# Kernel optimization log

Measured on AMD Instinct MI355X. Metric: run time of the kernel, lower is better.

Reference implementation:

```python
import jax, jax.numpy as jnp
import numpy as np

D = 64  # hidden size

def _ffn2(x, w1, b1, w2, b2):
    # Linear -> ReLU -> Linear (no activation after last layer, matching FFN)
    return jax.nn.relu(x @ w1 + b1) @ w2 + b2

def setup_inputs() -> dict:
    key = jax.random.key(0)
    ks = jax.random.split(key, 40)
    B, NP, NY, NO = 512, 128, 1024, 256
    f32 = jnp.float32
    def n(k, sh, s=0.1):
        return (jax.random.normal(k, sh) * s).astype(f32)
    inp = {
        'pred_state': jax.random.normal(ks[0], (B, NP, 2), dtype=f32),
        'prey_state': jax.random.normal(ks[1], (B, NY, 2), dtype=f32),
        'obst_state': jax.random.normal(ks[2], (B, NO, 3), dtype=f32),
        'prey_is_alive': jax.random.randint(ks[3], (B, NY), 0, 2).astype(bool),
        'emb': n(ks[4], (3, D)),
        'e0_w1': n(ks[5], (2, D)), 'e0_b1': n(ks[6], (D,)),
        'e0_w2': n(ks[7], (D, D)), 'e0_b2': n(ks[8], (D,)),
        'e1_w1': n(ks[9], (2, D)), 'e1_b1': n(ks[10], (D,)),
        'e1_w2': n(ks[11], (D, D)), 'e1_b2': n(ks[12], (D,)),
        'e2_w1': n(ks[13], (3, D)), 'e2_b1': n(ks[14], (D,)),
        'e2_w2': n(ks[15], (D, D)), 'e2_b2': n(ks[16], (D,)),
        'wq': n(ks[17], (D, D)), 'bq': n(ks[18], (D,)),
        'wk': n(ks[19], (D, D)), 'bk': n(ks[20], (D,)),
        'wv': n(ks[21], (D, D)), 'bv': n(ks[22], (D,)),
        'wp': n(ks[23], (2, D)), 'bp': n(ks[24], (D,)),
        'wo': n(ks[25], (D, D)), 'bo': n(ks[26], (D,)),
        'n_w1': n(ks[27], (D, D)), 'n_b1': n(ks[28], (D,)),
        'n_w2': n(ks[29], (D, D)), 'n_b2': n(ks[30], (D,)),
        'n_w3': n(ks[31], (D, 1), s=0.01), 'n_b3': n(ks[32], (1,)),
    }
    return inp

def reference(pred_state, prey_state, obst_state, prey_is_alive, emb,
              e0_w1, e0_b1, e0_w2, e0_b2,
              e1_w1, e1_b1, e1_w2, e1_b2,
              e2_w1, e2_b1, e2_w2, e2_b2,
              wq, bq, wk, bk, wv, bv, wp, bp, wo, bo,
              n_w1, n_b1, n_w2, n_b2, n_w3, n_b3):
    # per-entity encoders + type embedding
    x_pred = _ffn2(pred_state, e0_w1, e0_b1, e0_w2, e0_b2) + emb[0]  # [B,NP,D]
    x_prey = _ffn2(prey_state, e1_w1, e1_b1, e1_w2, e1_b2) + emb[1]  # [B,NY,D]
    x_obst = _ffn2(obst_state, e2_w1, e2_b1, e2_w2, e2_b2) + emb[2]  # [B,NO,D]
    x = jnp.concatenate([x_pred, x_prey, x_obst], axis=1)            # [B,N,D]
    pos = jnp.concatenate([pred_state, prey_state, obst_state[..., :2]], axis=1)  # [B,N,2]
    # NOTE: original mask = zeros.unsqueeze(-1) & (...) is identically False -> no masking.
    q = x_pred @ wq + bq   # [B,NP,D]
    k = x @ wk + bk        # [B,N,D]
    v = x @ wv + bv        # [B,N,D]
    # relative positional key bias: pbias = (pos_q - pos_k) @ wp; q . pbias folded as below
    qp = q @ wp.T          # [B,NP,2]
    scale = np.float32(1.0 / np.sqrt(D))
    scores = (jnp.einsum('bqd,bkd->bqk', q, k)
              + jnp.einsum('bqc,bqc->bq', qp, pred_state)[..., None]
              - jnp.einsum('bqc,bkc->bqk', qp, pos)
              + (q @ bp)[..., None]) * scale          # [B,NP,N]
    a = jax.nn.softmax(scores, axis=-1)
    out = jnp.einsum('bqk,bkd->bqd', a, v) @ wo + bo  # [B,NP,D]
    # output FFN with final Tanh
    h = jax.nn.relu(out @ n_w1 + n_b1)
    h = jax.nn.relu(h @ n_w2 + n_b2)
    return jnp.tanh(h @ n_w3 + n_b3)                  # [B,NP,1]
```

## Files before the change

kernel.cpp:

```cpp
#include <hip/hip_runtime.h>
#include <math.h>

#define NB 512
#define NPQ 128
#define NY 1024
#define NO 256
#define NTOT 1408

typedef __attribute__((ext_vector_type(8))) short bf16x8;
typedef __attribute__((ext_vector_type(4))) float f32x4;

__device__ __forceinline__ unsigned short f2bf(float f) {
    unsigned int u = __float_as_uint(f);
    u += 0x7fffu + ((u >> 16) & 1u);
    return (unsigned short)(u >> 16);
}
__device__ __forceinline__ float bf2f(short s) {
    return __uint_as_float(((unsigned int)(unsigned short)s) << 16);
}

union U8  { bf16x8 v; unsigned long long u[2]; };
union U16 { bf16x8 v; uint4 u; };

__global__ __launch_bounds__(256) void k_prepA(
    const float* __restrict__ emb,  const float* __restrict__ e0b2,
    const float* __restrict__ e0w2, const float* __restrict__ wq,
    const float* __restrict__ bq,   const float* __restrict__ wp,
    const float* __restrict__ bp,   const float* __restrict__ bk,
    const float* __restrict__ wvv,  const float* __restrict__ bv,
    const float* __restrict__ wo,   const float* __restrict__ bo,
    const float* __restrict__ e1b2, const float* __restrict__ e1w2,
    const float* __restrict__ e2b2, const float* __restrict__ e2w2,
    const float* __restrict__ nw1,  const float* __restrict__ nw2,
    float* __restrict__ W2qG, float* __restrict__ WvoG,
    float* __restrict__ scqG, float* __restrict__ b0g0,
    float* __restrict__ bvo,  float* __restrict__ BEP,
    unsigned short* __restrict__ W2P, unsigned short* __restrict__ WHP)
{
    const int tid = threadIdx.x, blk = blockIdx.x;

    if (blk < 16) {
        const int idx = blk*256 + tid;
        const int h = idx >> 6, j = idx & 63;
        float s0 = 0.f, s1 = 0.f, s2 = 0.f, s3 = 0.f;
        #pragma unroll 4
        for (int e = 0; e < 64; e += 4) {
            s0 = fmaf(e0w2[h*64+e],   wq[(e  )*64+j], s0);
            s1 = fmaf(e0w2[h*64+e+1], wq[(e+1)*64+j], s1);
            s2 = fmaf(e0w2[h*64+e+2], wq[(e+2)*64+j], s2);
            s3 = fmaf(e0w2[h*64+e+3], wq[(e+3)*64+j], s3);
        }
        W2qG[idx] = (s0 + s1) + (s2 + s3);
    } else if (blk < 32) {
        const int idx = (blk-16)*256 + tid;
        const int e = idx >> 6, o = idx & 63;
        float s0 = 0.f, s1 = 0.f, s2 = 0.f, s3 = 0.f;
        #pragma unroll 4
        for (int d = 0; d < 64; d += 4) {
            s0 = fmaf(wvv[e*64+d],   wo[(d  )*64+o], s0);
            s1 = fmaf(wvv[e*64+d+1], wo[(d+1)*64+o], s1);
            s2 = fmaf(wvv[e*64+d+2], wo[(d+2)*64+o], s2);
            s3 = fmaf(wvv[e*64+d+3], wo[(d+3)*64+o], s3);
        }
        WvoG[idx] = (s0 + s1) + (s2 + s3);
    } else if (blk < 38) {
        const int idx = (blk-32)*256 + tid;
        if (idx < 1536) {
            const int t = idx >> 9, rem = idx & 511;
            const int mt = rem >> 7, rem2 = rem & 127;
            const int kh = rem2 >> 6, lane = rem2 & 63;
            const int quad = lane >> 4, lq = lane & 15;
            const float* w2 = (t == 0) ? e0w2 : ((t == 1) ? e1w2 : e2w2);
            unsigned short v[8];
            #pragma unroll
            for (int j = 0; j < 8; ++j)
                v[j] = f2bf(w2[(kh*32 + quad*8 + j)*64 + mt*16 + lq]);
            *(uint4*)&W2P[(size_t)idx*8] = make_uint4(
                (unsigned int)v[0] | ((unsigned int)v[1] << 16),
                (unsigned int)v[2] | ((unsigned int)v[3] << 16),
                (unsigned int)v[4] | ((unsigned int)v[5] << 16),
                (unsigned int)v[6] | ((unsigned int)v[7] << 16));
        }
    } else if (blk < 42) {
        const int idx = 512 + (blk-38)*256 + tid;
        const int l = idx >> 9, rem = idx & 511;
        const int mt = rem >> 7, rem2 = rem & 127;
        const int kh = rem2 >> 6, lane = rem2 & 63;
        const int quad = lane >> 4, lq = lane & 15;
        const float* W = (l == 1) ? nw1 : nw2;
        unsigned short v[8];
        #pragma unroll
        for (int j = 0; j < 8; ++j)
            v[j] = f2bf(W[(kh*32 + quad*8 + j)*64 + mt*16 + lq]);
        *(uint4*)&WHP[(size_t)idx*8] = make_uint4(
            (unsigned int)v[0] | ((unsigned int)v[1] << 16),
            (unsigned int)v[2] | ((unsigned int)v[3] << 16),
            (unsigned int)v[4] | ((unsigned int)v[5] << 16),
            (unsigned int)v[6] | ((unsigned int)v[7] << 16));
    } else {
        __shared__ float scq[64];
        if (tid < 64) {
            const int j = tid;
            float s = bq[j];
            for (int e = 0; e < 64; ++e) s += (e0b2[e] + emb[e]) * wq[e*64+j];
            scq[j] = s;
            scqG[j] = s;
        }
        if (tid >= 64 && tid < 128) {
            const int o = tid - 64;
            float s = bo[o];
            for (int d = 0; d < 64; ++d) s += bv[d] * wo[d*64+o];
            bvo[o] = s;
        }
        {
            const int i = tid - 64;
            if (i >= 64 && i < 256) {
                const int idx = i - 64;
                const int t = idx >> 6, d = idx & 63;
                const float* b2 = (t == 0) ? e0b2 : ((t == 1) ? e1b2 : e2b2);
                BEP[idx] = b2[d] + emb[t*64 + d];
            }
        }
        __syncthreads();
        if (tid == 0) {
            float s0 = 0.f, s1 = 0.f, s2 = 0.f;
            for (int j = 0; j < 64; ++j) {
                s0 += scq[j] * wp[j];
                s1 += scq[j] * wp[64+j];
                s2 += scq[j] * (bp[j] + bk[j]);
            }
            b0g0[0] = s0; b0g0[1] = s1; b0g0[2] = s2;
        }
    }
}

__global__ __launch_bounds__(256) void k_prepB(
    const float* __restrict__ W2qG, const float* __restrict__ WvoG,
    const float* __restrict__ scqG,
    const float* __restrict__ wk, const float* __restrict__ wp,
    const float* __restrict__ bp, const float* __restrict__ bk,
    unsigned short* __restrict__ AqkP, unsigned short* __restrict__ P3P,
    float* __restrict__ a0, unsigned short* __restrict__ WHP)
{
    const int tid = threadIdx.x, blk = blockIdx.x;

    if (blk < 2) {
        const int idx = blk*256 + tid;
        const int fi = idx >> 6, lane = idx & 63;
        const int mt = fi >> 1, kh = fi & 1;
        const int quad = lane >> 4, lq = lane & 15;
        const int d = mt*16 + lq;
        unsigned short v[8];
        #pragma unroll
        for (int jj = 0; jj < 8; ++jj) {
            const int h = kh*32 + quad*8 + jj;
            float s0 = 0.f, s1 = 0.f, s2 = 0.f, s3 = 0.f;
            #pragma unroll 4
            for (int j = 0; j < 64; j += 4) {
                const float4 a = *(const float4*)&W2qG[h*64 + j];
                const float4 b = *(const float4*)&wk[d*64 + j];
                s0 = fmaf(a.x, b.x, s0); s1 = fmaf(a.y, b.y, s1);
                s2 = fmaf(a.z, b.z, s2); s3 = fmaf(a.w, b.w, s3);
            }
            v[jj] = f2bf((s0 + s1) + (s2 + s3));
        }
        *(uint4*)&AqkP[(size_t)idx*8] = make_uint4(
            (unsigned int)v[0] | ((unsigned int)v[1] << 16),
            (unsigned int)v[2] | ((unsigned int)v[3] << 16),
            (unsigned int)v[4] | ((unsigned int)v[5] << 16),
            (unsigned int)v[6] | ((unsigned int)v[7] << 16));
    } else if (blk == 2) {
        if (tid < 128) {
            const int idx = tid;
            const int kh = idx >> 6, lane = idx & 63;
            const int quad = lane >> 4, lq = lane & 15;
            unsigned short v[8];
            #pragma unroll
            for (int jj = 0; jj < 8; ++jj) {
                const int h = kh*32 + quad*8 + jj;
                float val = 0.f;
                if (lq == 0 || lq == 1) {
                    float s0 = 0.f, s1 = 0.f;
                    #pragma unroll 8
                    for (int j = 0; j < 64; j += 2) {
                        s0 = fmaf(W2qG[h*64+j],   wp[lq*64+j],   s0);
                        s1 = fmaf(W2qG[h*64+j+1], wp[lq*64+j+1], s1);
                    }
                    val = s0 + s1;
                } else if (lq == 2) {
                    float s0 = 0.f, s1 = 0.f;
                    #pragma unroll 8
                    for (int j = 0; j < 64; j += 2) {
                        s0 = fmaf(W2qG[h*64+j],   bp[j]   + bk[j],   s0);
                        s1 = fmaf(W2qG[h*64+j+1], bp[j+1] + bk[j+1], s1);
                    }
                    val = s0 + s1;
                }
                v[jj] = f2bf(val);
            }
            *(uint4*)&P3P[(size_t)idx*8] = make_uint4(
                (unsigned int)v[0] | ((unsigned int)v[1] << 16),
                (unsigned int)v[2] | ((unsigned int)v[3] << 16),
                (unsigned int)v[4] | ((unsigned int)v[5] << 16),
                (unsigned int)v[6] | ((unsigned int)v[7] << 16));
        } else if (tid < 192) {
            const int d = tid - 128;
            float s0 = 0.f, s1 = 0.f, s2 = 0.f, s3 = 0.f;
            #pragma unroll 4
            for (int j = 0; j < 64; j += 4) {
                const float4 a = *(const float4*)&scqG[j];
                const float4 b = *(const float4*)&wk[d*64 + j];
                s0 = fmaf(a.x, b.x, s0); s1 = fmaf(a.y, b.y, s1);
                s2 = fmaf(a.z, b.z, s2); s3 = fmaf(a.w, b.w, s3);
            }
            a0[d] = (s0 + s1) + (s2 + s3);
        }
    } else {
        #pragma unroll
        for (int pass = 0; pass < 2; ++pass) {
            const int idx = pass*256 + tid;
            const int mt = idx >> 7, rem2 = idx & 127;
            const int kh = rem2 >> 6, lane = rem2 & 63;
            const int quad = lane >> 4, lq = lane & 15;
            unsigned short v[8];
            #pragma unroll
            for (int j = 0; j < 8; ++j)
                v[j] = f2bf(WvoG[(kh*32 + quad*8 + j)*64 + mt*16 + lq]);
            *(uint4*)&WHP[(size_t)idx*8] = make_uint4(
                (unsigned int)v[0] | ((unsigned int)v[1] << 16),
                (unsigned int)v[2] | ((unsigned int)v[3] << 16),
                (unsigned int)v[4] | ((unsigned int)v[5] << 16),
                (unsigned int)v[6] | ((unsigned int)v[7] << 16));
        }
    }
}

__global__ __launch_bounds__(256) void k_encq(
    const float* __restrict__ pred, const float* __restrict__ prey,
    const float* __restrict__ obst,
    const unsigned short* __restrict__ W2P, const float* __restrict__ BEP,
    const float* __restrict__ e0w1, const float* __restrict__ e0b1,
    const float* __restrict__ e1w1, const float* __restrict__ e1b1,
    const float* __restrict__ e2w1, const float* __restrict__ e2b1,
    const unsigned short* __restrict__ AqkP, const float* __restrict__ a0,
    const unsigned short* __restrict__ P3P,  const float* __restrict__ b0g0,
    unsigned short* __restrict__ X, float* __restrict__ POS,
    float* __restrict__ QT, float* __restrict__ QP, float* __restrict__ QC)
{
    const int tid = threadIdx.x, lane = tid & 63, w = tid >> 6;
    const int lq = lane & 15, quad = lane >> 4;
    __shared__ __align__(16) short sH[4][32][68];

    if (blockIdx.x < 1408) {
        const int blk = blockIdx.x;
        int type, lrow0, cin, lsh, nmask, nbase;
        const float *st, *w1, *b1;
        if (blk < 128)       { type=0; lrow0=blk*512;         st=pred; w1=e0w1; b1=e0b1; cin=2; lsh=7;  nmask=NPQ-1; nbase=0; }
        else if (blk < 1152) { type=1; lrow0=(blk-128)*512;   st=prey; w1=e1w1; b1=e1b1; cin=2; lsh=10; nmask=NY-1;  nbase=NPQ; }
        else                 { type=2; lrow0=(blk-1152)*512;  st=obst; w1=e2w1; b1=e2b1; cin=3; lsh=8;  nmask=NO-1;  nbase=NPQ+NY; }

        bf16x8 wfrag[4][2];
        #pragma unroll
        for (int mt = 0; mt < 4; ++mt)
            #pragma unroll
            for (int kh = 0; kh < 2; ++kh)
                wfrag[mt][kh] = *(const bf16x8*)&W2P[(size_t)(((type*4 + mt)*2 + kh)*64 + lane)*8];

        float4 be[4];
        #pragma unroll
        for (int mt = 0; mt < 4; ++mt)
            be[mt] = *(const float4*)&BEP[type*64 + mt*16 + quad*4];

        float b1v[2][8], w0v[2][8], w1v[2][8], w2v[2][8];
        #pragma unroll
        for (int kh = 0; kh < 2; ++kh) {
            const int k0 = kh*32 + quad*8;
            *(float4*)&b1v[kh][0] = *(const float4*)&b1[k0];
            *(float4*)&b1v[kh][4] = *(const float4*)&b1[k0+4];
            *(float4*)&w0v[kh][0] = *(const float4*)&w1[k0];
            *(float4*)&w0v[kh][4] = *(const float4*)&w1[k0+4];
            *(float4*)&w1v[kh][0] = *(const float4*)&w1[64+k0];
            *(float4*)&w1v[kh][4] = *(const float4*)&w1[64+k0+4];
            if (cin == 3) {
                *(float4*)&w2v[kh][0] = *(const float4*)&w1[128+k0];
                *(float4*)&w2v[kh][4] = *(const float4*)&w1[128+k0+4];
            }
        }

        #pragma unroll
        for (int k = 0; k < 4; ++k) {
            const int i = tid*4 + k;
            const int r = i >> 1, c = i & 1;
            const int lr = lrow0 + r;
            const int pb = lr >> lsh, n = nbase + (lr & nmask);
            POS[((size_t)pb*NTOT + n)*2 + c] = st[(size_t)lr*cin + c];
        }

        for (int rt = 0; rt < 8; ++rt) {
            const int lr = lrow0 + w*128 + rt*16 + lq;
            float s0, s1, s2 = 0.f;
            if (cin == 2) {
                const float2 sv = *(const float2*)&st[(size_t)lr*2];
                s0 = sv.x; s1 = sv.y;
            } else {
                const float2 sv = *(const float2*)&st[(size_t)lr*3];
                s0 = sv.x; s1 = sv.y; s2 = st[(size_t)lr*3 + 2];
            }
            bf16x8 hb[2];
            #pragma unroll
            for (int kh = 0; kh < 2; ++kh)
                #pragma unroll
                for (int j = 0; j < 8; ++j) {
                    float a = b1v[kh][j] + s0*w0v[kh][j] + s1*w1v[kh][j];
                    if (cin == 3) a += s2*w2v[kh][j];
                    hb[kh][j] = (short)f2bf(fmaxf(a, 0.f));
                }

            f32x4 acc[4];
            #pragma unroll
            for (int mt = 0; mt < 4; ++mt) acc[mt] = (f32x4){0.f,0.f,0.f,0.f};
            #pragma unroll
            for (int mt = 0; mt < 4; ++mt) {
                acc[mt] = __builtin_amdgcn_mfma_f32_16x16x32_bf16(wfrag[mt][0], hb[0], acc[mt], 0, 0, 0);
                acc[mt] = __builtin_amdgcn_mfma_f32_16x16x32_bf16(wfrag[mt][1], hb[1], acc[mt], 0, 0, 0);
            }

            const int bb = lr >> lsh, n = nbase + (lr & nmask);
            unsigned short* xbase = X + ((size_t)bb*NTOT + n)*64;
            #pragma unroll
            for (int mt = 0; mt < 4; ++mt) {
                const unsigned int u0 = (unsigned int)f2bf(acc[mt][0] + be[mt].x)
                                      | ((unsigned int)f2bf(acc[mt][1] + be[mt].y) << 16);
                const unsigned int u1 = (unsigned int)f2bf(acc[mt][2] + be[mt].z)
                                      | ((unsigned int)f2bf(acc[mt][3] + be[mt].w) << 16);
                *(uint2*)(xbase + mt*16 + quad*4) = make_uint2(u0, u1);
            }
        }
    } else {
        const int b = blockIdx.x - 1408;
        const float w1r0 = e0w1[lane], w1r1 = e0w1[64+lane], b1r = e0b1[lane];
        {
            const float* sp = pred + ((size_t)b*NPQ + w*32)*2;
            #pragma unroll
            for (int r = 0; r < 32; ++r) {
                const float a = b1r + sp[2*r]*w1r0 + sp[2*r+1]*w1r1;
                sH[w][r][lane] = (short)f2bf(fmaxf(a, 0.f));
            }
        }

        bf16x8 wfrag[4][2], a3[2];
        #pragma unroll
        for (int mt = 0; mt < 4; ++mt)
            #pragma unroll
            for (int kh = 0; kh < 2; ++kh)
                wfrag[mt][kh] = *(const bf16x8*)&AqkP[(size_t)((mt*2 + kh)*64 + lane)*8];
        #pragma unroll
        for (int kh = 0; kh < 2; ++kh)
            a3[kh] = *(const bf16x8*)&P3P[(size_t)(kh*64 + lane)*8];

        float4 a0r[4];
        #pragma unroll
        for (int mt = 0; mt < 4; ++mt) a0r[mt] = *(const float4*)&a0[mt*16 + quad*4];
        const float c0 = b0g0[0], c1 = b0g0[1], c2 = b0g0[2];

        __syncthreads();

        for (int bt = 0; bt < 2; ++bt) {
            U8 hb0, hb1;
            const short* hp = &sH[w][bt*16 + lq][0];
            hb0.u[0] = *(const unsigned long long*)(hp + quad*8);
            hb0.u[1] = *(const unsigned long long*)(hp + quad*8 + 4);
            hb1.u[0] = *(const unsigned long long*)(hp + 32 + quad*8);
            hb1.u[1] = *(const unsigned long long*)(hp + 32 + quad*8 + 4);

            f32x4 acc[4], acc3;
            #pragma unroll
            for (int mt = 0; mt < 4; ++mt) acc[mt] = (f32x4){0.f,0.f,0.f,0.f};
            acc3 = (f32x4){0.f,0.f,0.f,0.f};
            #pragma unroll
            for (int mt = 0; mt < 4; ++mt) {
                acc[mt] = __builtin_amdgcn_mfma_f32_16x16x32_bf16(wfrag[mt][0], hb0.v, acc[mt], 0, 0, 0);
                acc[mt] = __builtin_amdgcn_mfma_f32_16x16x32_bf16(wfrag[mt][1], hb1.v, acc[mt], 0, 0, 0);
            }
            acc3 = __builtin_amdgcn_mfma_f32_16x16x32_bf16(a3[0], hb0.v, acc3, 0, 0, 0);
            acc3 = __builtin_amdgcn_mfma_f32_16x16x32_bf16(a3[1], hb1.v, acc3, 0, 0, 0);

            const int row = b*NPQ + w*32 + bt*16 + lq;
            #pragma unroll
            for (int mt = 0; mt < 4; ++mt) {
                *(float4*)&QT[(size_t)row*64 + mt*16 + quad*4] = make_float4(
                    acc[mt][0] + a0r[mt].x, acc[mt][1] + a0r[mt].y,
                    acc[mt][2] + a0r[mt].z, acc[mt][3] + a0r[mt].w);
            }
            if (quad == 0) {
                const float qp0 = acc3[0] + c0, qp1 = acc3[1] + c1, qs = acc3[2] + c2;
                const float p0 = pred[(size_t)row*2], p1 = pred[(size_t)row*2 + 1];
                QP[(size_t)row*2]     = qp0;
                QP[(size_t)row*2 + 1] = qp1;
                QC[row] = qp0*p0 + qp1*p1 + qs;
            }
        }
    }
}

__global__ __launch_bounds__(256, 2) void k_attn(
    const unsigned short* __restrict__ X, const float* __restrict__ POS,
    const float* __restrict__ QT, const float* __restrict__ QP,
    const float* __restrict__ QC,
    const unsigned short* __restrict__ WHP,
    const float* __restrict__ bvo, const float* __restrict__ nb1,
    const float* __restrict__ nb2,
    const float* __restrict__ nw3, const float* __restrict__ nb3,
    float* __restrict__ OUT)
{
    const int tid = threadIdx.x, b = blockIdx.x;
    const int w = tid >> 6, lane = tid & 63, lq = lane & 15, quad = lane >> 4;

    __shared__ __align__(16) short sXc[2][64][68];
    __shared__ __align__(16) short sP[4][32][68];
    __shared__ __align__(16) short sA[128][68];
    __shared__ __align__(16) short sB[128][68];
    __shared__ float sw3[64];

    bf16x8 aq[2][2];
    #pragma unroll
    for (int qt = 0; qt < 2; ++qt) {
        const float* qrow = QT + ((size_t)b*NPQ + w*32 + qt*16 + lq)*64;
        #pragma unroll
        for (int kh = 0; kh < 2; ++kh)
            #pragma unroll
            for (int j = 0; j < 8; ++j)
                aq[qt][kh][j] = (short)f2bf(qrow[kh*32 + quad*8 + j]);
    }

    float qcr[2][4], qp0r[2][4], qp1r[2][4], lacc[2][4];
    f32x4 O[2][4];
    #pragma unroll
    for (int qt = 0; qt < 2; ++qt)
        #pragma unroll
        for (int i = 0; i < 4; ++i) {
            const size_t g = (size_t)b*NPQ + w*32 + qt*16 + quad*4 + i;
            qcr[qt][i]  = QC[g];
            qp0r[qt][i] = -QP[2*g];
            qp1r[qt][i] = -QP[2*g+1];
            lacc[qt][i] = 0.f;
        }
    #pragma unroll
    for (int qt = 0; qt < 2; ++qt)
        #pragma unroll
        for (int nt = 0; nt < 4; ++nt) O[qt][nt] = (f32x4){0.f,0.f,0.f,0.f};
    const float E = 0.180336884f;

    const int skey = tid & 63, sd0 = (tid >> 6) * 16;

    for (int kt = 0; kt < 22; ++kt) {
        const int par = kt & 1;

        const unsigned short* gx = X + ((size_t)b*NTOT + kt*64 + skey)*64 + sd0;
        const uint4 t0 = *(const uint4*)(gx);
        const uint4 t1 = *(const uint4*)(gx + 8);

        if (kt > 0) {
            const int pb = par ^ 1;
            #pragma unroll
            for (int kc = 0; kc < 2; ++kc) {
                U8 pa[2];
                #pragma unroll
                for (int qt = 0; qt < 2; ++qt) {
                    const short* pp = &sP[w][qt*16 + lq][kc*32 + quad*8];
                    pa[qt].u[0] = *(const unsigned long long*)pp;
                    pa[qt].u[1] = *(const unsigned long long*)(pp + 4);
                }
                #pragma unroll
                for (int nt = 0; nt < 4; ++nt) {
                    U8 bv;
                    const short* xp = &sXc[pb][nt*16 + lq][kc*32 + quad*8];
                    bv.u[0] = *(const unsigned long long*)xp;
                    bv.u[1] = *(const unsigned long long*)(xp + 4);
                    O[0][nt] = __builtin_amdgcn_mfma_f32_16x16x32_bf16(pa[0].v, bv.v, O[0][nt], 0, 0, 0);
                    O[1][nt] = __builtin_amdgcn_mfma_f32_16x16x32_bf16(pa[1].v, bv.v, O[1][nt], 0, 0, 0);
                }
            }
        }

        __builtin_amdgcn_sched_barrier(0);

        #pragma unroll
        for (int nt = 0; nt < 4; ++nt) {
            U16 bx0, bx1;
            const unsigned short* xrow = X + ((size_t)b*NTOT + kt*64 + nt*16 + lq)*64;
            bx0.u = *(const uint4*)(xrow + quad*8);
            bx1.u = *(const uint4*)(xrow + 32 + quad*8);
            const float pos0 = POS[((size_t)b*NTOT + kt*64 + nt*16 + lq)*2];
            const float pos1 = POS[((size_t)b*NTOT + kt*64 + nt*16 + lq)*2 + 1];
            #pragma unroll
            for (int qt = 0; qt < 2; ++qt) {
                f32x4 sa = (f32x4){0.f,0.f,0.f,0.f};
                sa = __builtin_amdgcn_mfma_f32_16x16x32_bf16(aq[qt][0], bx0.v, sa, 0, 0, 0);
                sa = __builtin_amdgcn_mfma_f32_16x16x32_bf16(aq[qt][1], bx1.v, sa, 0, 0, 0);
                #pragma unroll
                for (int i = 0; i < 4; ++i) {
                    float s = sa[i] + qcr[qt][i];
                    s = fmaf(qp0r[qt][i], pos0, s);
                    s = fmaf(qp1r[qt][i], pos1, s);
                    const float p = exp2f(s * E);
                    lacc[qt][i] += p;
                    sP[w][qt*16 + quad*4 + i][nt*16 + lq] = (short)f2bf(p);
                }
            }
        }

        {
            unsigned short tmp[16];
            *(uint4*)tmp = t0; *(uint4*)(tmp+8) = t1;
            #pragma unroll
            for (int j = 0; j < 16; ++j) sXc[par][sd0+j][skey] = (short)tmp[j];
        }

        __syncthreads();
    }

    {
        #pragma unroll
        for (int kc = 0; kc < 2; ++kc) {
            U8 pa[2];
            #pragma unroll
            for (int qt = 0; qt < 2; ++qt) {
                const short* pp = &sP[w][qt*16 + lq][kc*32 + quad*8];
                pa[qt].u[0] = *(const unsigned long long*)pp;
                pa[qt].u[1] = *(const unsigned long long*)(pp + 4);
            }
            #pragma unroll
            for (int nt = 0; nt < 4; ++nt) {
                U8 bv;
                const short* xp = &sXc[1][nt*16 + lq][kc*32 + quad*8];
                bv.u[0] = *(const unsigned long long*)xp;
                bv.u[1] = *(const unsigned long long*)(xp + 4);
                O[0][nt] = __builtin_amdgcn_mfma_f32_16x16x32_bf16(pa[0].v, bv.v, O[0][nt], 0, 0, 0);
                O[1][nt] = __builtin_amdgcn_mfma_f32_16x16x32_bf16(pa[1].v, bv.v, O[1][nt], 0, 0, 0);
            }
        }
    }

    #pragma unroll
    for (int qt = 0; qt < 2; ++qt)
        #pragma unroll
        for (int i = 0; i < 4; ++i) {
            #pragma unroll
            for (int off = 1; off < 16; off <<= 1)
                lacc[qt][i] += __shfl_xor(lacc[qt][i], off);
            const float rl = 1.f / lacc[qt][i];
            const int row = w*32 + qt*16 + quad*4 + i;
            #pragma unroll
            for (int nt = 0; nt < 4; ++nt)
                sA[row][nt*16 + lq] = (short)f2bf(O[qt][nt][i] * rl);
        }
    if (tid < 64) sw3[tid] = nw3[tid];
    __syncthreads();

    const float* Bs[3] = {bvo, nb1, nb2};
    for (int l = 0; l < 3; ++l) {
        bf16x8 wfrag[4][2];
        #pragma unroll
        for (int mt = 0; mt < 4; ++mt)
            #pragma unroll
            for (int kh = 0; kh < 2; ++kh)
                wfrag[mt][kh] = *(const bf16x8*)&WHP[(size_t)(((l*4 + mt)*2 + kh)*64 + lane)*8];
        const float* Bb = Bs[l];
        float be[4][4];
        #pragma unroll
        for (int mt = 0; mt < 4; ++mt)
            #pragma unroll
            for (int i = 0; i < 4; ++i) be[mt][i] = Bb[mt*16 + quad*4 + i];

        short (*src)[68] = (l & 1) ? sB : sA;
        short (*dst)[68] = (l & 1) ? sA : sB;
        const bool doRelu = (l >= 1);

        for (int bt = 0; bt < 2; ++bt) {
            U8 hb0, hb1;
            const short* hp = &src[w*32 + bt*16 + lq][0];
            hb0.u[0] = *(const unsigned long long*)(hp + quad*8);
            hb0.u[1] = *(const unsigned long long*)(hp + quad*8 + 4);
            hb1.u[0] = *(const unsigned long long*)(hp + 32 + quad*8);
            hb1.u[1] = *(const unsigned long long*)(hp + 32 + quad*8 + 4);

            f32x4 acc[4];
            #pragma unroll
            for (int mt = 0; mt < 4; ++mt) acc[mt] = (f32x4){0.f,0.f,0.f,0.f};
            #pragma unroll
            for (int mt = 0; mt < 4; ++mt) {
                acc[mt] = __builtin_amdgcn_mfma_f32_16x16x32_bf16(wfrag[mt][0], hb0.v, acc[mt], 0, 0, 0);
                acc[mt] = __builtin_amdgcn_mfma_f32_16x16x32_bf16(wfrag[mt][1], hb1.v, acc[mt], 0, 0, 0);
            }
            const int row = w*32 + bt*16 + lq;
            #pragma unroll
            for (int mt = 0; mt < 4; ++mt) {
                float v0 = acc[mt][0] + be[mt][0];
                float v1 = acc[mt][1] + be[mt][1];
                float v2 = acc[mt][2] + be[mt][2];
                float v3 = acc[mt][3] + be[mt][3];
                if (doRelu) {
                    v0 = fmaxf(v0, 0.f); v1 = fmaxf(v1, 0.f);
                    v2 = fmaxf(v2, 0.f); v3 = fmaxf(v3, 0.f);
                }
                const unsigned int u0 = (unsigned int)f2bf(v0) | ((unsigned int)f2bf(v1) << 16);
                const unsigned int u1 = (unsigned int)f2bf(v2) | ((unsigned int)f2bf(v3) << 16);
                *(uint2*)&dst[row][mt*16 + quad*4] = make_uint2(u0, u1);
            }
        }
        __syncthreads();
    }

    if (tid < 128) {
        const int row = tid;
        float acc = nb3[0];
        #pragma unroll 16
        for (int d = 0; d < 64; ++d) acc += bf2f(sB[row][d]) * sw3[d];
        OUT[(size_t)b*NPQ + row] = tanhf(acc);
    }
}

extern "C" void kernel_launch(void* const* d_in, const int* in_sizes, int n_in,
                              void* d_out, int out_size, void* d_ws, size_t ws_size,
                              hipStream_t stream)
{
    const float* pred = (const float*)d_in[0];
    const float* prey = (const float*)d_in[1];
    const float* obst = (const float*)d_in[2];
    const float* emb  = (const float*)d_in[4];
    const float* e0w1 = (const float*)d_in[5];
    const float* e0b1 = (const float*)d_in[6];
    const float* e0w2 = (const float*)d_in[7];
    const float* e0b2 = (const float*)d_in[8];
    const float* e1w1 = (const float*)d_in[9];
    const float* e1b1 = (const float*)d_in[10];
    const float* e1w2 = (const float*)d_in[11];
    const float* e1b2 = (const float*)d_in[12];
    const float* e2w1 = (const float*)d_in[13];
    const float* e2b1 = (const float*)d_in[14];
    const float* e2w2 = (const float*)d_in[15];
    const float* e2b2 = (const float*)d_in[16];
    const float* wq  = (const float*)d_in[17];
    const float* bq  = (const float*)d_in[18];
    const float* wk  = (const float*)d_in[19];
    const float* bk  = (const float*)d_in[20];
    const float* wvv = (const float*)d_in[21];
    const float* bv  = (const float*)d_in[22];
    const float* wp  = (const float*)d_in[23];
    const float* bp  = (const float*)d_in[24];
    const float* wo  = (const float*)d_in[25];
    const float* bo  = (const float*)d_in[26];
    const float* nw1 = (const float*)d_in[27];
    const float* nb1 = (const float*)d_in[28];
    const float* nw2 = (const float*)d_in[29];
    const float* nb2 = (const float*)d_in[30];
    const float* nw3 = (const float*)d_in[31];
    const float* nb3 = (const float*)d_in[32];

    char* ws = (char*)d_ws;
    unsigned short* X = (unsigned short*)ws;
    float* F    = (float*)(ws + 92274688);
    float* POS  = F;
    float* QT   = POS + 1441792;
    float* QP   = QT  + 4194304;
    float* QC   = QP  + 131072;
    float* a0   = QC  + 65536;
    float* b0g0 = a0  + 64;
    float* bvo  = b0g0 + 4;
    float* BEP  = bvo + 64;
    float* W2qG = BEP + 192;
    float* WvoG = W2qG + 4096;
    float* scqG = WvoG + 4096;
    unsigned short* W2P  = (unsigned short*)(scqG + 64);
    unsigned short* AqkP = W2P + 12288;
    unsigned short* P3P  = AqkP + 4096;
    unsigned short* WHP  = P3P + 1024;

    k_prepA<<<43, 256, 0, stream>>>(emb, e0b2, e0w2, wq, bq, wp, bp, bk,
        wvv, bv, wo, bo, e1b2, e1w2, e2b2, e2w2, nw1, nw2,
        W2qG, WvoG, scqG, b0g0, bvo, BEP, W2P, WHP);
    k_prepB<<<4, 256, 0, stream>>>(W2qG, WvoG, scqG, wk, wp, bp, bk,
        AqkP, P3P, a0, WHP);
    k_encq<<<1920, 256, 0, stream>>>(pred, prey, obst, W2P, BEP,
        e0w1, e0b1, e1w1, e1b1, e2w1, e2b1,
        AqkP, a0, P3P, b0g0, X, POS, QT, QP, QC);
    k_attn<<<512, 256, 0, stream>>>(X, POS, QT, QP, QC,
        WHP, bvo, nb1, nb2, nw3, nb3, (float*)d_out);
}
```

Before: 248.0 us.

## Split attention kernel across two blocks per batch over query halves

Measured after the change: 324.2 us. +30.7%, slower.

```diff
diff --git a/kernel.cpp b/kernel.cpp
--- a/kernel.cpp
+++ b/kernel.cpp
@@ -403,7 +403,7 @@
     }
 }
 
-__global__ __launch_bounds__(256, 2) void k_attn(
+__global__ __launch_bounds__(256, 3) void k_attn(
     const unsigned short* __restrict__ X, const float* __restrict__ POS,
     const float* __restrict__ QT, const float* __restrict__ QP,
     const float* __restrict__ QC,
@@ -413,42 +413,38 @@
     const float* __restrict__ nw3, const float* __restrict__ nb3,
     float* __restrict__ OUT)
 {
-    const int tid = threadIdx.x, b = blockIdx.x;
+    const int tid = threadIdx.x;
+    const int b = blockIdx.x >> 1, qh = blockIdx.x & 1;
     const int w = tid >> 6, lane = tid & 63, lq = lane & 15, quad = lane >> 4;
+    const int qbase = qh*64 + w*16;
 
     __shared__ __align__(16) short sXc[2][64][68];
-    __shared__ __align__(16) short sP[4][32][68];
-    __shared__ __align__(16) short sA[128][68];
-    __shared__ __align__(16) short sB[128][68];
+    __shared__ __align__(16) short sP[4][16][68];
+    __shared__ __align__(16) short sA[64][68];
+    __shared__ __align__(16) short sB[64][68];
     __shared__ float sw3[64];
 
-    bf16x8 aq[2][2];
+    bf16x8 aq[2];
+    {
+        const float* qrow = QT + ((size_t)b*NPQ + qbase + lq)*64;
+        #pragma unroll
+        for (int kh = 0; kh < 2; ++kh)
+            #pragma unroll
+            for (int j = 0; j < 8; ++j)
+                aq[kh][j] = (short)f2bf(qrow[kh*32 + quad*8 + j]);
+    }
+
+    float qcr[4], qp0r[4], qp1r[4], lacc[4];
+    f32x4 O[4];
     #pragma unroll
-    for (int qt = 0; qt < 2; ++qt) {
-        const float* qrow = QT + ((size_t)b*NPQ + w*32 + qt*16 + lq)*64;
-        #pragma unroll
-        for (int kh = 0; kh < 2; ++kh)
-            #pragma unroll
-            for (int j = 0; j < 8; ++j)
-                aq[qt][kh][j] = (short)f2bf(qrow[kh*32 + quad*8 + j]);
-    }
-
-    float qcr[2][4], qp0r[2][4], qp1r[2][4], lacc[2][4];
-    f32x4 O[2][4];
-    #pragma unroll
-    for (int qt = 0; qt < 2; ++qt)
-        #pragma unroll
-        for (int i = 0; i < 4; ++i) {
-            const size_t g = (size_t)b*NPQ + w*32 + qt*16 + quad*4 + i;
-            qcr[qt][i]  = QC[g];
-            qp0r[qt][i] = -QP[2*g];
-            qp1r[qt][i] = -QP[2*g+1];
-            lacc[qt][i] = 0.f;
-        }
-    #pragma unroll
-    for (int qt = 0; qt < 2; ++qt)
-        #pragma unroll
-        for (int nt = 0; nt < 4; ++nt) O[qt][nt] = (f32x4){0.f,0.f,0.f,0.f};
+    for (int i = 0; i < 4; ++i) {
+        const size_t g = (size_t)b*NPQ + qbase + quad*4 + i;
+        qcr[i]  = QC[g];
+        qp0r[i] = -QP[2*g];
+        qp1r[i] = -QP[2*g+1];
+        lacc[i] = 0.f;
+        O[i] = (f32x4){0.f, 0.f, 0.f, 0.f};
+    }
     const float E = 0.180336884f;
 
     const int skey = tid & 63, sd0 = (tid >> 6) * 16;
@@ -464,21 +460,17 @@
             const int pb = par ^ 1;
             #pragma unroll
             for (int kc = 0; kc < 2; ++kc) {
-                U8 pa[2];
-                #pragma unroll
-                for (int qt = 0; qt < 2; ++qt) {
-                    const short* pp = &sP[w][qt*16 + lq][kc*32 + quad*8];
-                    pa[qt].u[0] = *(const unsigned long long*)pp;
-                    pa[qt].u[1] = *(const unsigned long long*)(pp + 4);
-                }
+                U8 pa;
+                const short* pp = &sP[w][lq][kc*32 + quad*8];
+                pa.u[0] = *(const unsigned long long*)pp;
+                pa.u[1] = *(const unsigned long long*)(pp + 4);
                 #pragma unroll
                 for (int nt = 0; nt < 4; ++nt) {
                     U8 bv;
                     const short* xp = &sXc[pb][nt*16 + lq][kc*32 + quad*8];
                     bv.u[0] = *(const unsigned long long*)xp;
                     bv.u[1] = *(const unsigned long long*)(xp + 4);
-                    O[0][nt] = __builtin_amdgcn_mfma_f32_16x16x32_bf16(pa[0].v, bv.v, O[0][nt], 0, 0, 0);
-                    O[1][nt] = __builtin_amdgcn_mfma_f32_16x16x32_bf16(pa[1].v, bv.v, O[1][nt], 0, 0, 0);
+                    O[nt] = __builtin_amdgcn_mfma_f32_16x16x32_bf16(pa.v, bv.v, O[nt], 0, 0, 0);
                 }
             }
         }
@@ -493,20 +485,17 @@
             bx1.u = *(const uint4*)(xrow + 32 + quad*8);
             const float pos0 = POS[((size_t)b*NTOT + kt*64 + nt*16 + lq)*2];
             const float pos1 = POS[((size_t)b*NTOT + kt*64 + nt*16 + lq)*2 + 1];
-            #pragma unroll
-            for (int qt = 0; qt < 2; ++qt) {
-                f32x4 sa = (f32x4){0.f,0.f,0.f,0.f};
-                sa = __builtin_amdgcn_mfma_f32_16x16x32_bf16(aq[qt][0], bx0.v, sa, 0, 0, 0);
-                sa = __builtin_amdgcn_mfma_f32_16x16x32_bf16(aq[qt][1], bx1.v, sa, 0, 0, 0);
-                #pragma unroll
-                for (int i = 0; i < 4; ++i) {
-                    float s = sa[i] + qcr[qt][i];
-                    s = fmaf(qp0r[qt][i], pos0, s);
-                    s = fmaf(qp1r[qt][i], pos1, s);
-                    const float p = exp2f(s * E);
-                    lacc[qt][i] += p;
-                    sP[w][qt*16 + quad*4 + i][nt*16 + lq] = (short)f2bf(p);
-                }
+            f32x4 sa = (f32x4){0.f,0.f,0.f,0.f};
+            sa = __builtin_amdgcn_mfma_f32_16x16x32_bf16(aq[0], bx0.v, sa, 0, 0, 0);
+            sa = __builtin_amdgcn_mfma_f32_16x16x32_bf16(aq[1], bx1.v, sa, 0, 0, 0);
+            #pragma unroll
+            for (int i = 0; i < 4; ++i) {
+                float s = sa[i] + qcr[i];
+                s = fmaf(qp0r[i], pos0, s);
+                s = fmaf(qp1r[i], pos1, s);
+                const float p = exp2f(s * E);
+                lacc[i] += p;
+                sP[w][quad*4 + i][nt*16 + lq] = (short)f2bf(p);
             }
         }
 
@@ -523,38 +512,32 @@
     {
         #pragma unroll
         for (int kc = 0; kc < 2; ++kc) {
-            U8 pa[2];
-            #pragma unroll
-            for (int qt = 0; qt < 2; ++qt) {
-                const short* pp = &sP[w][qt*16 + lq][kc*32 + quad*8];
-                pa[qt].u[0] = *(const unsigned long long*)pp;
-                pa[qt].u[1] = *(const unsigned long long*)(pp + 4);
-            }
+            U8 pa;
+            const short* pp = &sP[w][lq][kc*32 + quad*8];
+            pa.u[0] = *(const unsigned long long*)pp;
+            pa.u[1] = *(const unsigned long long*)(pp + 4);
             #pragma unroll
             for (int nt = 0; nt < 4; ++nt) {
                 U8 bv;
                 const short* xp = &sXc[1][nt*16 + lq][kc*32 + quad*8];
                 bv.u[0] = *(const unsigned long long*)xp;
                 bv.u[1] = *(const unsigned long long*)(xp + 4);
-                O[0][nt] = __builtin_amdgcn_mfma_f32_16x16x32_bf16(pa[0].v, bv.v, O[0][nt], 0, 0, 0);
-                O[1][nt] = __builtin_amdgcn_mfma_f32_16x16x32_bf16(pa[1].v, bv.v, O[1][nt], 0, 0, 0);
+                O[nt] = __builtin_amdgcn_mfma_f32_16x16x32_bf16(pa.v, bv.v, O[nt], 0, 0, 0);
             }
         }
     }
 
     #pragma unroll
-    for (int qt = 0; qt < 2; ++qt)
-        #pragma unroll
-        for (int i = 0; i < 4; ++i) {
-            #pragma unroll
-            for (int off = 1; off < 16; off <<= 1)
-                lacc[qt][i] += __shfl_xor(lacc[qt][i], off);
-            const float rl = 1.f / lacc[qt][i];
-            const int row = w*32 + qt*16 + quad*4 + i;
-            #pragma unroll
-            for (int nt = 0; nt < 4; ++nt)
-                sA[row][nt*16 + lq] = (short)f2bf(O[qt][nt][i] * rl);
-        }
+    for (int i = 0; i < 4; ++i) {
+        #pragma unroll
+        for (int off = 1; off < 16; off <<= 1)
+            lacc[i] += __shfl_xor(lacc[i], off);
+        const float rl = 1.f / lacc[i];
+        const int row = w*16 + quad*4 + i;
+        #pragma unroll
+        for (int nt = 0; nt < 4; ++nt)
+            sA[row][nt*16 + lq] = (short)f2bf(O[nt][i] * rl);
+    }
     if (tid < 64) sw3[tid] = nw3[tid];
     __syncthreads();
 
@@ -577,9 +560,9 @@
         short (*dst)[68] = (l & 1) ? sA : sB;
         const bool doRelu = (l >= 1);
 
-        for (int bt = 0; bt < 2; ++bt) {
+        {
             U8 hb0, hb1;
-            const short* hp = &src[w*32 + bt*16 + lq][0];
+            const short* hp = &src[w*16 + lq][0];
             hb0.u[0] = *(const unsigned long long*)(hp + quad*8);
             hb0.u[1] = *(const unsigned long long*)(hp + quad*8 + 4);
             hb1.u[0] = *(const unsigned long long*)(hp + 32 + quad*8);
@@ -593,7 +576,7 @@
                 acc[mt] = __builtin_amdgcn_mfma_f32_16x16x32_bf16(wfrag[mt][0], hb0.v, acc[mt], 0, 0, 0);
                 acc[mt] = __builtin_amdgcn_mfma_f32_16x16x32_bf16(wfrag[mt][1], hb1.v, acc[mt], 0, 0, 0);
             }
-            const int row = w*32 + bt*16 + lq;
+            const int row = w*16 + lq;
             #pragma unroll
             for (int mt = 0; mt < 4; ++mt) {
                 float v0 = acc[mt][0] + be[mt][0];
@@ -612,12 +595,12 @@
         __syncthreads();
     }
 
-    if (tid < 128) {
+    if (tid < 64) {
         const int row = tid;
         float acc = nb3[0];
         #pragma unroll 16
         for (int d = 0; d < 64; ++d) acc += bf2f(sB[row][d]) * sw3[d];
-        OUT[(size_t)b*NPQ + row] = tanhf(acc);
+        OUT[(size_t)b*NPQ + qh*64 + row] = tanhf(acc);
     }
 }
 
@@ -685,6 +668,6 @@
     k_encq<<<1920, 256, 0, stream>>>(pred, prey, obst, W2P, BEP,
         e0w1, e0b1, e1w1, e1b1, e2w1, e2b1,
         AqkP, a0, P3P, b0g0, X, POS, QT, QP, QC);
-    k_attn<<<512, 256, 0, stream>>>(X, POS, QT, QP, QC,
+    k_attn<<<1024, 256, 0, stream>>>(X, POS, QT, QP, QC,
         WHP, bvo, nb1, nb2, nw3, nb3, (float*)d_out);
 }
```
